# Kernel optimization log

Hardware: AMD Instinct MI355X
Metric: run time of the kernel (lower is better)

The kernel has to match this reference:

```python
import jax, jax.numpy as jnp
import numpy as np

S = 4096      # total packed tokens
B = 8         # number of variable-length segments
E = 1152      # embed_dim (SigLIP2 so400m)
H = 16        # num_heads
D = E // H    # head_dim = 72


def setup_inputs() -> dict:
    key = jax.random.key(0)
    ks = jax.random.split(key, 8)
    w_std = 0.02
    theta = jax.random.uniform(ks[1], (S, D), jnp.float32, 0.0, 2.0 * np.pi)
    return {
        "hidden_states": jax.random.normal(ks[0], (S, E), jnp.float32),
        "cu_seqlens": jnp.arange(B + 1, dtype=jnp.int32) * (S // B),
        "cos": jnp.cos(theta),
        "sin": jnp.sin(theta),
        "Wq": jax.random.normal(ks[2], (E, E), jnp.float32) * w_std,
        "bq": jnp.zeros((E,), jnp.float32),
        "Wk": jax.random.normal(ks[3], (E, E), jnp.float32) * w_std,
        "bk": jnp.zeros((E,), jnp.float32),
        "Wv": jax.random.normal(ks[4], (E, E), jnp.float32) * w_std,
        "bv": jnp.zeros((E,), jnp.float32),
        "Wo": jax.random.normal(ks[5], (E, E), jnp.float32) * w_std,
        "bo": jnp.zeros((E,), jnp.float32),
    }


def _rotate_half(x):
    x1, x2 = jnp.split(x, 2, axis=-1)
    return jnp.concatenate((-x2, x1), axis=-1)


def reference(hidden_states, cu_seqlens, cos, sin, Wq, bq, Wk, bk, Wv, bv, Wo, bo):
    seq_len = hidden_states.shape[0]
    scale = np.float32(D) ** -0.5
    # projections -> [S, H, D]
    q = (hidden_states @ Wq.T + bq).reshape(seq_len, H, D)
    k = (hidden_states @ Wk.T + bk).reshape(seq_len, H, D)
    v = (hidden_states @ Wv.T + bv).reshape(seq_len, H, D)
    # inline RoPE (apply_rotary_pos_emb_vision): cos/sin broadcast over heads
    c = cos[:, None, :]
    s = sin[:, None, :]
    q = q * c + _rotate_half(q) * s
    k = k * c + _rotate_half(k) * s
    # segment id per token from cu_seqlens; block-diagonal attention mask
    seg = jnp.searchsorted(cu_seqlens[1:], jnp.arange(seq_len, dtype=cu_seqlens.dtype), side="right")
    mask = seg[:, None] == seg[None, :]                     # [S, S]
    scores = jnp.einsum("shd,thd->hst", q, k) * scale       # [H, S, S]
    neg = jnp.finfo(scores.dtype).min
    scores = jnp.where(mask[None, :, :], scores, neg)
    probs = jax.nn.softmax(scores, axis=-1)
    attn = jnp.einsum("hst,thd->shd", probs, v).reshape(seq_len, E)
    return attn @ Wo.T + bo
```

## Files before the change

### kernel.cpp

```cpp
#include <hip/hip_runtime.h>
#include <float.h>

#define S_LEN 4096
#define E_DIM 1152
#define NH    16
#define HD    72
#define HD2   36
#define NQKV  3456

typedef __attribute__((ext_vector_type(4))) float f32x4;
typedef __attribute__((ext_vector_type(8))) _Float16 f16x8;

__device__ __forceinline__ unsigned short f2h(float f) {
    union { _Float16 h; unsigned short u; } c;
    c.h = (_Float16)f;
    return c.u;
}

__device__ __forceinline__ void gload_lds16(const unsigned short* g, unsigned short* l) {
    __builtin_amdgcn_global_load_lds(
        (const __attribute__((address_space(1))) unsigned int*)g,
        (__attribute__((address_space(3))) unsigned int*)l, 16, 0, 0);
}

__global__ __launch_bounds__(256)
void pack_f16(const float* __restrict__ hs, const float* __restrict__ wq,
              const float* __restrict__ wk, const float* __restrict__ wv,
              const float* __restrict__ wo,
              unsigned short* __restrict__ hs_h, unsigned short* __restrict__ wqkv_h,
              unsigned short* __restrict__ wo_h)
{
    const float* src; unsigned short* dst; int n4;
    const int WSZ = E_DIM * E_DIM;
    switch (blockIdx.z) {
        case 0: src = hs; dst = hs_h;             n4 = S_LEN * E_DIM / 4; break;
        case 1: src = wq; dst = wqkv_h;           n4 = WSZ / 4; break;
        case 2: src = wk; dst = wqkv_h + WSZ;     n4 = WSZ / 4; break;
        case 3: src = wv; dst = wqkv_h + 2 * WSZ; n4 = WSZ / 4; break;
        default: src = wo; dst = wo_h;            n4 = WSZ / 4; break;
    }
    for (int i = blockIdx.x * 256 + threadIdx.x; i < n4; i += gridDim.x * 256) {
        f32x4 x = ((const f32x4*)src)[i];
        ushort4 hv;
        hv.x = f2h(x[0]); hv.y = f2h(x[1]); hv.z = f2h(x[2]); hv.w = f2h(x[3]);
        ((ushort4*)dst)[i] = hv;
    }
}

__global__ __launch_bounds__(256, 4)
void gemm_qkv_f16(const unsigned short* __restrict__ Ah, const unsigned short* __restrict__ Wh,
                  const float* __restrict__ bq, const float* __restrict__ bk,
                  const float* __restrict__ bv,
                  float* __restrict__ oq, float* __restrict__ ok, float* __restrict__ ov)
{
    __shared__ unsigned short sA[128 * 64];
    __shared__ unsigned short sB[128 * 64];
    const int tid  = threadIdx.x;
    const int w    = tid >> 6, lane = tid & 63;
    const int quad = lane >> 4, m = lane & 15;
    const int wr   = w & 1,  wc = w >> 1;

    const int bid = blockIdx.x;
    const int lin = (bid & 7) * 108 + (bid >> 3);
    const int n_t = lin >> 5;
    const int m_t = lin & 31;
    const int m0  = m_t * 128;
    const int n0  = n_t * 128;

    const int srow = lane >> 3;
    const int skc  = (lane & 7) ^ srow;

    f32x4 acc[4][4];
    #pragma unroll
    for (int i = 0; i < 4; ++i)
        #pragma unroll
        for (int j = 0; j < 4; ++j) acc[i][j] = (f32x4){0.f, 0.f, 0.f, 0.f};

    const int rm7 = m & 7;

    for (int k0 = 0; k0 < E_DIM; k0 += 64) {
        #pragma unroll
        for (int c = 0; c < 4; ++c) {
            int r = 32 * w + 8 * c + srow;
            gload_lds16(Ah + (size_t)(m0 + r) * E_DIM + k0 + skc * 8, &sA[(32 * w + 8 * c) * 64]);
            gload_lds16(Wh + (size_t)(n0 + r) * E_DIM + k0 + skc * 8, &sB[(32 * w + 8 * c) * 64]);
        }
        __syncthreads();

        #pragma unroll
        for (int k3 = 0; k3 < 2; ++k3) {
            f16x8 ah[4], bh[4];
            #pragma unroll
            for (int t = 0; t < 4; ++t) {
                int pc = ((k3 << 2) + quad) ^ rm7;
                ah[t] = *(const f16x8*)&sA[(64 * wr + 16 * t + m) * 64 + pc * 8];
                bh[t] = *(const f16x8*)&sB[(64 * wc + 16 * t + m) * 64 + pc * 8];
            }
            #pragma unroll
            for (int rt = 0; rt < 4; ++rt)
                #pragma unroll
                for (int ct = 0; ct < 4; ++ct)
                    acc[rt][ct] = __builtin_amdgcn_mfma_f32_16x16x32_f16(ah[rt], bh[ct], acc[rt][ct], 0, 0, 0);
        }
        __syncthreads();
    }

    const int which = n0 / E_DIM;
    const int n0l = n0 - which * E_DIM;
    const float* bp = (which == 0) ? bq : (which == 1) ? bk : bv;
    float* Cp       = (which == 0) ? oq : (which == 1) ? ok : ov;
    #pragma unroll
    for (int ct = 0; ct < 4; ++ct) {
        int col = n0l + 64 * wc + 16 * ct + m;
        float bias = bp[col];
        #pragma unroll
        for (int rt = 0; rt < 4; ++rt)
            #pragma unroll
            for (int reg = 0; reg < 4; ++reg) {
                int row = m0 + 64 * wr + 16 * rt + 4 * quad + reg;
                Cp[(size_t)row * E_DIM + col] = acc[rt][ct][reg] + bias;
            }
    }
}

__global__ __launch_bounds__(256, 4)
void gemm_out_f16(const unsigned short* __restrict__ Ah, const unsigned short* __restrict__ Wh,
                  const float* __restrict__ bo, float* __restrict__ Cp)
{
    __shared__ unsigned short sA[64 * 64];
    __shared__ unsigned short sB[128 * 64];
    const int tid  = threadIdx.x;
    const int w    = tid >> 6, lane = tid & 63;
    const int quad = lane >> 4, m = lane & 15;
    const int m0   = blockIdx.y * 64;
    const int n0   = blockIdx.x * 128;

    const int srow = lane >> 3;
    const int skc  = (lane & 7) ^ srow;

    f32x4 acc[4][2];
    #pragma unroll
    for (int i = 0; i < 4; ++i)
        #pragma unroll
        for (int j = 0; j < 2; ++j) acc[i][j] = (f32x4){0.f, 0.f, 0.f, 0.f};

    const int rm7 = m & 7;

    for (int k0 = 0; k0 < E_DIM; k0 += 64) {
        #pragma unroll
        for (int c = 0; c < 2; ++c) {
            int r = 16 * w + 8 * c + srow;
            gload_lds16(Ah + (size_t)(m0 + r) * E_DIM + k0 + skc * 8, &sA[(16 * w + 8 * c) * 64]);
        }
        #pragma unroll
        for (int c = 0; c < 4; ++c) {
            int r = 32 * w + 8 * c + srow;
            gload_lds16(Wh + (size_t)(n0 + r) * E_DIM + k0 + skc * 8, &sB[(32 * w + 8 * c) * 64]);
        }
        __syncthreads();
        #pragma unroll
        for (int k3 = 0; k3 < 2; ++k3) {
            f16x8 ah[4], bh[2];
            int pc = ((k3 << 2) + quad) ^ rm7;
            #pragma unroll
            for (int t = 0; t < 4; ++t)
                ah[t] = *(const f16x8*)&sA[(16 * t + m) * 64 + pc * 8];
            #pragma unroll
            for (int ct = 0; ct < 2; ++ct)
                bh[ct] = *(const f16x8*)&sB[(32 * w + 16 * ct + m) * 64 + pc * 8];
            #pragma unroll
            for (int rt = 0; rt < 4; ++rt)
                #pragma unroll
                for (int ct = 0; ct < 2; ++ct)
                    acc[rt][ct] = __builtin_amdgcn_mfma_f32_16x16x32_f16(ah[rt], bh[ct], acc[rt][ct], 0, 0, 0);
        }
        __syncthreads();
    }

    #pragma unroll
    for (int ct = 0; ct < 2; ++ct) {
        int col = n0 + 32 * w + 16 * ct + m;
        float bias = bo[col];
        #pragma unroll
        for (int rt = 0; rt < 4; ++rt)
            #pragma unroll
            for (int reg = 0; reg < 4; ++reg) {
                int row = m0 + 16 * rt + 4 * quad + reg;
                Cp[(size_t)row * E_DIM + col] = acc[rt][ct][reg] + bias;
            }
    }
}

__global__ __launch_bounds__(256)
void vtrans(const float* __restrict__ v, unsigned short* __restrict__ vt)
{
    __shared__ unsigned short tile[HD][72];
    const int h = blockIdx.y;
    const int s0 = blockIdx.x * 64;
    for (int task = threadIdx.x; task < 64 * 18; task += 256) {
        int r = task / 18, c = task % 18;
        f32x4 x = *(const f32x4*)(v + (size_t)(s0 + r) * E_DIM + h * HD + (c << 2));
        tile[(c << 2) + 0][r] = f2h(x[0]);
        tile[(c << 2) + 1][r] = f2h(x[1]);
        tile[(c << 2) + 2][r] = f2h(x[2]);
        tile[(c << 2) + 3][r] = f2h(x[3]);
    }
    __syncthreads();
    for (int task = threadIdx.x; task < HD * 8; task += 256) {
        int d = task / 8, cc = task % 8;
        uint4 val = *(const uint4*)&tile[d][cc << 3];
        *(uint4*)(vt + ((size_t)h * HD + d) * S_LEN + s0 + (cc << 3)) = val;
    }
}

__global__ __launch_bounds__(256, 4)
void attn_rope(const float* __restrict__ qf, const float* __restrict__ kf,
               const float* __restrict__ cosb, const float* __restrict__ sinb,
               const unsigned short* __restrict__ vt, const int* __restrict__ cu,
               int nseg, unsigned short* __restrict__ out)
{
    __shared__ unsigned short ks_s[64][72];
    __shared__ unsigned short vs_s[80][72];
    __shared__ unsigned short ss_s[64][72];

    const int tid  = threadIdx.x;
    const int w    = tid >> 6;
    const int lane = tid & 63;
    const int quad = lane >> 4;
    const int m    = lane & 15;
    const int h    = blockIdx.y;
    const int qb0  = blockIdx.x * 64;
    const float scale = 0.11785113019775793f;

    {
        uint4 zz = make_uint4(0u, 0u, 0u, 0u);
        if (tid < 72) {
            int r = 72 + tid / 9, c = tid % 9;
            *(uint4*)&vs_s[r][c << 3] = zz;
        }
    }

    int rs_r[4], re_r[4];
    #pragma unroll
    for (int reg = 0; reg < 4; ++reg) {
        int row = qb0 + 16 * w + 4 * quad + reg;
        int st = 0;
        for (int i = 1; i < nseg; ++i) if (cu[i] <= row) st = i;
        rs_r[reg] = cu[st];
        re_r[reg] = cu[st + 1];
    }
    int st0 = 0, st1 = 0;
    for (int i = 1; i < nseg; ++i) {
        if (cu[i] <= qb0) st0 = i;
        if (cu[i] <= qb0 + 63) st1 = i;
    }
    const int kstart = cu[st0];
    const int kend   = cu[st1 + 1];

    for (int task = tid; task < 64 * 9; task += 256) {
        int row = task / 9, d0 = (task % 9) << 2;
        int s = qb0 + row;
        const float* xr = qf + (size_t)s * E_DIM + h * HD;
        f32x4 a  = *(const f32x4*)(xr + d0);
        f32x4 b  = *(const f32x4*)(xr + d0 + HD2);
        f32x4 c1 = *(const f32x4*)(cosb + (size_t)s * HD + d0);
        f32x4 s1 = *(const f32x4*)(sinb + (size_t)s * HD + d0);
        f32x4 c2 = *(const f32x4*)(cosb + (size_t)s * HD + d0 + HD2);
        f32x4 s2 = *(const f32x4*)(sinb + (size_t)s * HD + d0 + HD2);
        f32x4 r1 = a * c1 - b * s1;
        f32x4 r2 = b * c2 + a * s2;
        uint2 u1, u2;
        u1.x = (unsigned)f2h(r1[0]) | ((unsigned)f2h(r1[1]) << 16);
        u1.y = (unsigned)f2h(r1[2]) | ((unsigned)f2h(r1[3]) << 16);
        u2.x = (unsigned)f2h(r2[0]) | ((unsigned)f2h(r2[1]) << 16);
        u2.y = (unsigned)f2h(r2[2]) | ((unsigned)f2h(r2[3]) << 16);
        *(uint2*)&ks_s[row][d0]       = u1;
        *(uint2*)&ks_s[row][d0 + HD2] = u2;
    }
    __syncthreads();

    f16x8 qfr[3];
    {
        const unsigned short* qrow = &ks_s[16 * w + m][0];
        #pragma unroll
        for (int k3 = 0; k3 < 3; ++k3) {
            bool pad = (k3 == 2) && (quad != 0);
            int off = pad ? 0 : (k3 * 32 + quad * 8);
            f16x8 val = *(const f16x8*)(qrow + off);
            f16x8 z = {0, 0, 0, 0, 0, 0, 0, 0};
            qfr[k3] = pad ? z : val;
        }
    }

    f32x4 acc_o[5];
    #pragma unroll
    for (int i = 0; i < 5; ++i) acc_o[i] = (f32x4){0.f, 0.f, 0.f, 0.f};
    float l_r[4] = {0.f, 0.f, 0.f, 0.f};

    for (int kb_i = kstart; kb_i < kend; kb_i += 64) {
        __syncthreads();
        for (int task = tid; task < 64 * 9; task += 256) {
            int row = task / 9, d0 = (task % 9) << 2;
            int s = kb_i + row; if (s >= kend) s = kend - 1;
            const float* xr = kf + (size_t)s * E_DIM + h * HD;
            f32x4 a  = *(const f32x4*)(xr + d0);
            f32x4 b  = *(const f32x4*)(xr + d0 + HD2);
            f32x4 c1 = *(const f32x4*)(cosb + (size_t)s * HD + d0);
            f32x4 s1 = *(const f32x4*)(sinb + (size_t)s * HD + d0);
            f32x4 c2 = *(const f32x4*)(cosb + (size_t)s * HD + d0 + HD2);
            f32x4 s2 = *(const f32x4*)(sinb + (size_t)s * HD + d0 + HD2);
            f32x4 r1 = a * c1 - b * s1;
            f32x4 r2 = b * c2 + a * s2;
            uint2 u1, u2;
            u1.x = (unsigned)f2h(r1[0]) | ((unsigned)f2h(r1[1]) << 16);
            u1.y = (unsigned)f2h(r1[2]) | ((unsigned)f2h(r1[3]) << 16);
            u2.x = (unsigned)f2h(r2[0]) | ((unsigned)f2h(r2[1]) << 16);
            u2.y = (unsigned)f2h(r2[2]) | ((unsigned)f2h(r2[3]) << 16);
            *(uint2*)&ks_s[row][d0]       = u1;
            *(uint2*)&ks_s[row][d0 + HD2] = u2;
        }
        for (int slot = tid; slot < 72 * 8; slot += 256) {
            int d = slot / 8, c = slot % 8;
            int kk0 = kb_i + (c << 3);
            if (kk0 > S_LEN - 8) kk0 = S_LEN - 8;
            uint4 val = *(const uint4*)(vt + ((size_t)h * HD + d) * S_LEN + kk0);
            *(uint4*)&vs_s[d][c << 3] = val;
        }
        __syncthreads();

        f32x4 sacc[4];
        #pragma unroll
        for (int ct = 0; ct < 4; ++ct) sacc[ct] = (f32x4){0.f, 0.f, 0.f, 0.f};
        #pragma unroll
        for (int ct = 0; ct < 4; ++ct) {
            const unsigned short* krow = &ks_s[16 * ct + m][0];
            #pragma unroll
            for (int k3 = 0; k3 < 3; ++k3) {
                bool pad = (k3 == 2) && (quad != 0);
                int off = pad ? 0 : (k3 * 32 + quad * 8);
                f16x8 bfr = *(const f16x8*)(krow + off);
                f16x8 z = {0, 0, 0, 0, 0, 0, 0, 0};
                bfr = pad ? z : bfr;
                sacc[ct] = __builtin_amdgcn_mfma_f32_16x16x32_f16(qfr[k3], bfr, sacc[ct], 0, 0, 0);
            }
        }

        #pragma unroll
        for (int ct = 0; ct < 4; ++ct) {
            int key = kb_i + 16 * ct + m;
            #pragma unroll
            for (int reg = 0; reg < 4; ++reg) {
                bool valid = (key >= rs_r[reg]) && (key < re_r[reg]);
                float p = valid ? __expf(sacc[ct][reg] * scale) : 0.f;
                l_r[reg] += p;
                ss_s[16 * w + 4 * quad + reg][16 * ct + m] = f2h(p);
            }
        }

        {
            const unsigned short* prow = &ss_s[16 * w + m][0];
            f16x8 pf0 = *(const f16x8*)(prow + quad * 8);
            f16x8 pf1 = *(const f16x8*)(prow + 32 + quad * 8);
            #pragma unroll
            for (int ct2 = 0; ct2 < 5; ++ct2) {
                const unsigned short* vrow = &vs_s[16 * ct2 + m][0];
                f16x8 vf0 = *(const f16x8*)(vrow + quad * 8);
                f16x8 vf1 = *(const f16x8*)(vrow + 32 + quad * 8);
                acc_o[ct2] = __builtin_amdgcn_mfma_f32_16x16x32_f16(pf0, vf0, acc_o[ct2], 0, 0, 0);
                acc_o[ct2] = __builtin_amdgcn_mfma_f32_16x16x32_f16(pf1, vf1, acc_o[ct2], 0, 0, 0);
            }
        }
    }

    #pragma unroll
    for (int reg = 0; reg < 4; ++reg) {
        float l = l_r[reg];
        l += __shfl_xor(l, 1);
        l += __shfl_xor(l, 2);
        l += __shfl_xor(l, 4);
        l += __shfl_xor(l, 8);
        l_r[reg] = l;
    }

    #pragma unroll
    for (int reg = 0; reg < 4; ++reg) {
        float linv = (l_r[reg] > 0.f) ? 1.f / l_r[reg] : 0.f;
        int row = qb0 + 16 * w + 4 * quad + reg;
        unsigned short* orow = out + (size_t)row * E_DIM + h * HD;
        #pragma unroll
        for (int ct2 = 0; ct2 < 5; ++ct2) {
            int col = 16 * ct2 + m;
            if (col < HD) orow[col] = f2h(acc_o[ct2][reg] * linv);
        }
    }
}

extern "C" void kernel_launch(void* const* d_in, const int* in_sizes, int n_in,
                              void* d_out, int out_size, void* d_ws, size_t ws_size,
                              hipStream_t stream)
{
    const float* hs   = (const float*)d_in[0];
    const int*   cu   = (const int*)d_in[1];
    const float* cosb = (const float*)d_in[2];
    const float* sinb = (const float*)d_in[3];
    const float* Wq   = (const float*)d_in[4];
    const float* bq   = (const float*)d_in[5];
    const float* Wk   = (const float*)d_in[6];
    const float* bk   = (const float*)d_in[7];
    const float* Wv   = (const float*)d_in[8];
    const float* bv   = (const float*)d_in[9];
    const float* Wo   = (const float*)d_in[10];
    const float* bo   = (const float*)d_in[11];
    float* outp = (float*)d_out;

    const size_t mat = (size_t)S_LEN * E_DIM;
    float* qf = (float*)d_ws;
    float* kf = qf + mat;
    float* vf = kf + mat;
    unsigned short* hs_h   = (unsigned short*)(vf + mat);
    unsigned short* wqkv_h = hs_h + mat;
    unsigned short* wo_h   = wqkv_h + (size_t)NQKV * E_DIM;
    unsigned short* vtb    = wo_h + (size_t)E_DIM * E_DIM;
    unsigned short* attn_h = hs_h;

    const int nseg = in_sizes[1] - 1;

    dim3 gpack(512, 1, 5);
    pack_f16<<<gpack, 256, 0, stream>>>(hs, Wq, Wk, Wv, Wo, hs_h, wqkv_h, wo_h);

    gemm_qkv_f16<<<dim3(864), 256, 0, stream>>>(hs_h, wqkv_h, bq, bk, bv, qf, kf, vf);

    dim3 gvt(S_LEN / 64, NH, 1);
    vtrans<<<gvt, 256, 0, stream>>>(vf, vtb);

    dim3 gattn(S_LEN / 64, NH, 1);
    attn_rope<<<gattn, 256, 0, stream>>>(qf, kf, cosb, sinb, vtb, cu, nseg, attn_h);

    dim3 gout(E_DIM / 128, S_LEN / 64, 1);
    gemm_out_f16<<<gout, 256, 0, stream>>>(attn_h, wo_h, bo, outp);
}
```

Before: 227.5 us.

## Precompute RoPE'd fp16 K, register-prefetch K/V tiles, fast exp2 softmax

```diff
diff --git a/kernel.cpp b/kernel.cpp
--- a/kernel.cpp
+++ b/kernel.cpp
@@ -192,32 +192,59 @@
 }
 
 __global__ __launch_bounds__(256)
-void vtrans(const float* __restrict__ v, unsigned short* __restrict__ vt)
+void prep_kv(const float* __restrict__ kf, const float* __restrict__ vf,
+             const float* __restrict__ cosb, const float* __restrict__ sinb,
+             unsigned short* __restrict__ kh, unsigned short* __restrict__ vt)
 {
     __shared__ unsigned short tile[HD][72];
-    const int h = blockIdx.y;
+    const int h  = blockIdx.y;
     const int s0 = blockIdx.x * 64;
-    for (int task = threadIdx.x; task < 64 * 18; task += 256) {
-        int r = task / 18, c = task % 18;
-        f32x4 x = *(const f32x4*)(v + (size_t)(s0 + r) * E_DIM + h * HD + (c << 2));
-        tile[(c << 2) + 0][r] = f2h(x[0]);
-        tile[(c << 2) + 1][r] = f2h(x[1]);
-        tile[(c << 2) + 2][r] = f2h(x[2]);
-        tile[(c << 2) + 3][r] = f2h(x[3]);
-    }
-    __syncthreads();
-    for (int task = threadIdx.x; task < HD * 8; task += 256) {
-        int d = task / 8, cc = task % 8;
-        uint4 val = *(const uint4*)&tile[d][cc << 3];
-        *(uint4*)(vt + ((size_t)h * HD + d) * S_LEN + s0 + (cc << 3)) = val;
+
+    if (blockIdx.z == 0) {
+        for (int task = threadIdx.x; task < 64 * 9; task += 256) {
+            int row = task / 9, d0 = (task % 9) << 2;
+            int s = s0 + row;
+            const float* xr = kf + (size_t)s * E_DIM + h * HD;
+            f32x4 a  = *(const f32x4*)(xr + d0);
+            f32x4 b  = *(const f32x4*)(xr + d0 + HD2);
+            f32x4 c1 = *(const f32x4*)(cosb + (size_t)s * HD + d0);
+            f32x4 s1 = *(const f32x4*)(sinb + (size_t)s * HD + d0);
+            f32x4 c2 = *(const f32x4*)(cosb + (size_t)s * HD + d0 + HD2);
+            f32x4 s2 = *(const f32x4*)(sinb + (size_t)s * HD + d0 + HD2);
+            f32x4 r1 = a * c1 - b * s1;
+            f32x4 r2 = b * c2 + a * s2;
+            uint2 u1, u2;
+            u1.x = (unsigned)f2h(r1[0]) | ((unsigned)f2h(r1[1]) << 16);
+            u1.y = (unsigned)f2h(r1[2]) | ((unsigned)f2h(r1[3]) << 16);
+            u2.x = (unsigned)f2h(r2[0]) | ((unsigned)f2h(r2[1]) << 16);
+            u2.y = (unsigned)f2h(r2[2]) | ((unsigned)f2h(r2[3]) << 16);
+            unsigned short* orow = kh + ((size_t)h * S_LEN + s) * HD;
+            *(uint2*)&orow[d0]       = u1;
+            *(uint2*)&orow[d0 + HD2] = u2;
+        }
+    } else {
+        for (int task = threadIdx.x; task < 64 * 18; task += 256) {
+            int r = task / 18, c = task % 18;
+            f32x4 x = *(const f32x4*)(vf + (size_t)(s0 + r) * E_DIM + h * HD + (c << 2));
+            tile[(c << 2) + 0][r] = f2h(x[0]);
+            tile[(c << 2) + 1][r] = f2h(x[1]);
+            tile[(c << 2) + 2][r] = f2h(x[2]);
+            tile[(c << 2) + 3][r] = f2h(x[3]);
+        }
+        __syncthreads();
+        for (int task = threadIdx.x; task < HD * 8; task += 256) {
+            int d = task / 8, cc = task % 8;
+            uint4 val = *(const uint4*)&tile[d][cc << 3];
+            *(uint4*)(vt + ((size_t)h * HD + d) * S_LEN + s0 + (cc << 3)) = val;
+        }
     }
 }
 
 __global__ __launch_bounds__(256, 4)
-void attn_rope(const float* __restrict__ qf, const float* __restrict__ kf,
-               const float* __restrict__ cosb, const float* __restrict__ sinb,
-               const unsigned short* __restrict__ vt, const int* __restrict__ cu,
-               int nseg, unsigned short* __restrict__ out)
+void attn_f16(const float* __restrict__ qf, const float* __restrict__ cosb,
+              const float* __restrict__ sinb, const unsigned short* __restrict__ kh,
+              const unsigned short* __restrict__ vt, const int* __restrict__ cu,
+              int nseg, unsigned short* __restrict__ out)
 {
     __shared__ unsigned short ks_s[64][72];
     __shared__ unsigned short vs_s[80][72];
@@ -230,7 +257,7 @@
     const int m    = lane & 15;
     const int h    = blockIdx.y;
     const int qb0  = blockIdx.x * 64;
-    const float scale = 0.11785113019775793f;
+    const float cexp = 0.17002324f;
 
     {
         uint4 zz = make_uint4(0u, 0u, 0u, 0u);
@@ -256,6 +283,28 @@
     }
     const int kstart = cu[st0];
     const int kend   = cu[st1 + 1];
+    const bool aligned = (st0 == st1);
+
+    const unsigned short* ktbase = kh + (size_t)h * S_LEN * HD;
+    const unsigned short* vtbase = vt + (size_t)h * HD * S_LEN;
+    unsigned short* ksf = &ks_s[0][0];
+
+    const int sl0 = tid, sl1 = tid + 256;
+    const int sl2 = (tid < 64) ? tid + 512 : tid + 256;
+    const int vd0 = sl0 >> 3, vc0 = (sl0 & 7) << 3;
+    const int vd1 = sl1 >> 3, vc1 = (sl1 & 7) << 3;
+    const int vd2 = sl2 >> 3, vc2 = (sl2 & 7) << 3;
+
+    uint4 kp0, kp1, kp2, vp0, vp1, vp2;
+    {
+        const unsigned short* kt = ktbase + (size_t)kstart * HD;
+        kp0 = *(const uint4*)(kt + sl0 * 8);
+        kp1 = *(const uint4*)(kt + sl1 * 8);
+        kp2 = *(const uint4*)(kt + sl2 * 8);
+        vp0 = *(const uint4*)(vtbase + (size_t)vd0 * S_LEN + kstart + vc0);
+        vp1 = *(const uint4*)(vtbase + (size_t)vd1 * S_LEN + kstart + vc1);
+        vp2 = *(const uint4*)(vtbase + (size_t)vd2 * S_LEN + kstart + vc2);
+    }
 
     for (int task = tid; task < 64 * 9; task += 256) {
         int row = task / 9, d0 = (task % 9) << 2;
@@ -297,36 +346,26 @@
     for (int i = 0; i < 5; ++i) acc_o[i] = (f32x4){0.f, 0.f, 0.f, 0.f};
     float l_r[4] = {0.f, 0.f, 0.f, 0.f};
 
-    for (int kb_i = kstart; kb_i < kend; kb_i += 64) {
-        __syncthreads();
-        for (int task = tid; task < 64 * 9; task += 256) {
-            int row = task / 9, d0 = (task % 9) << 2;
-            int s = kb_i + row; if (s >= kend) s = kend - 1;
-            const float* xr = kf + (size_t)s * E_DIM + h * HD;
-            f32x4 a  = *(const f32x4*)(xr + d0);
-            f32x4 b  = *(const f32x4*)(xr + d0 + HD2);
-            f32x4 c1 = *(const f32x4*)(cosb + (size_t)s * HD + d0);
-            f32x4 s1 = *(const f32x4*)(sinb + (size_t)s * HD + d0);
-            f32x4 c2 = *(const f32x4*)(cosb + (size_t)s * HD + d0 + HD2);
-            f32x4 s2 = *(const f32x4*)(sinb + (size_t)s * HD + d0 + HD2);
-            f32x4 r1 = a * c1 - b * s1;
-            f32x4 r2 = b * c2 + a * s2;
-            uint2 u1, u2;
-            u1.x = (unsigned)f2h(r1[0]) | ((unsigned)f2h(r1[1]) << 16);
-            u1.y = (unsigned)f2h(r1[2]) | ((unsigned)f2h(r1[3]) << 16);
-            u2.x = (unsigned)f2h(r2[0]) | ((unsigned)f2h(r2[1]) << 16);
-            u2.y = (unsigned)f2h(r2[2]) | ((unsigned)f2h(r2[3]) << 16);
-            *(uint2*)&ks_s[row][d0]       = u1;
-            *(uint2*)&ks_s[row][d0 + HD2] = u2;
-        }
-        for (int slot = tid; slot < 72 * 8; slot += 256) {
-            int d = slot / 8, c = slot % 8;
-            int kk0 = kb_i + (c << 3);
-            if (kk0 > S_LEN - 8) kk0 = S_LEN - 8;
-            uint4 val = *(const uint4*)(vt + ((size_t)h * HD + d) * S_LEN + kk0);
-            *(uint4*)&vs_s[d][c << 3] = val;
-        }
-        __syncthreads();
+    for (int kb = kstart; kb < kend; kb += 64) {
+        __syncthreads();
+        *(uint4*)(ksf + sl0 * 8) = kp0;
+        *(uint4*)(ksf + sl1 * 8) = kp1;
+        if (tid < 64) *(uint4*)(ksf + sl2 * 8) = kp2;
+        *(uint4*)&vs_s[vd0][vc0] = vp0;
+        *(uint4*)&vs_s[vd1][vc1] = vp1;
+        if (tid < 64) *(uint4*)&vs_s[vd2][vc2] = vp2;
+        __syncthreads();
+
+        int kn = kb + 64;
+        if (kn < kend) {
+            const unsigned short* kt = ktbase + (size_t)kn * HD;
+            kp0 = *(const uint4*)(kt + sl0 * 8);
+            kp1 = *(const uint4*)(kt + sl1 * 8);
+            kp2 = *(const uint4*)(kt + sl2 * 8);
+            vp0 = *(const uint4*)(vtbase + (size_t)vd0 * S_LEN + kn + vc0);
+            vp1 = *(const uint4*)(vtbase + (size_t)vd1 * S_LEN + kn + vc1);
+            vp2 = *(const uint4*)(vtbase + (size_t)vd2 * S_LEN + kn + vc2);
+        }
 
         f32x4 sacc[4];
         #pragma unroll
@@ -345,15 +384,26 @@
             }
         }
 
-        #pragma unroll
-        for (int ct = 0; ct < 4; ++ct) {
-            int key = kb_i + 16 * ct + m;
-            #pragma unroll
-            for (int reg = 0; reg < 4; ++reg) {
-                bool valid = (key >= rs_r[reg]) && (key < re_r[reg]);
-                float p = valid ? __expf(sacc[ct][reg] * scale) : 0.f;
-                l_r[reg] += p;
-                ss_s[16 * w + 4 * quad + reg][16 * ct + m] = f2h(p);
+        if (aligned) {
+            #pragma unroll
+            for (int ct = 0; ct < 4; ++ct)
+                #pragma unroll
+                for (int reg = 0; reg < 4; ++reg) {
+                    float p = __builtin_amdgcn_exp2f(sacc[ct][reg] * cexp);
+                    l_r[reg] += p;
+                    ss_s[16 * w + 4 * quad + reg][16 * ct + m] = f2h(p);
+                }
+        } else {
+            #pragma unroll
+            for (int ct = 0; ct < 4; ++ct) {
+                int key = kb + 16 * ct + m;
+                #pragma unroll
+                for (int reg = 0; reg < 4; ++reg) {
+                    bool valid = (key >= rs_r[reg]) && (key < re_r[reg]);
+                    float p = valid ? __builtin_amdgcn_exp2f(sacc[ct][reg] * cexp) : 0.f;
+                    l_r[reg] += p;
+                    ss_s[16 * w + 4 * quad + reg][16 * ct + m] = f2h(p);
+                }
             }
         }
 
@@ -421,7 +471,8 @@
     unsigned short* wqkv_h = hs_h + mat;
     unsigned short* wo_h   = wqkv_h + (size_t)NQKV * E_DIM;
     unsigned short* vtb    = wo_h + (size_t)E_DIM * E_DIM;
-    unsigned short* attn_h = hs_h;
+    unsigned short* kh     = hs_h;
+    unsigned short* attn_h = (unsigned short*)vf;
 
     const int nseg = in_sizes[1] - 1;
 
@@ -430,11 +481,11 @@
 
     gemm_qkv_f16<<<dim3(864), 256, 0, stream>>>(hs_h, wqkv_h, bq, bk, bv, qf, kf, vf);
 
-    dim3 gvt(S_LEN / 64, NH, 1);
-    vtrans<<<gvt, 256, 0, stream>>>(vf, vtb);
+    dim3 gprep(S_LEN / 64, NH, 2);
+    prep_kv<<<gprep, 256, 0, stream>>>(kf, vf, cosb, sinb, kh, vtb);
 
     dim3 gattn(S_LEN / 64, NH, 1);
-    attn_rope<<<gattn, 256, 0, stream>>>(qf, kf, cosb, sinb, vtb, cu, nseg, attn_h);
+    attn_f16<<<gattn, 256, 0, stream>>>(qf, cosb, sinb, kh, vtb, cu, nseg, attn_h);
 
     dim3 gout(E_DIM / 128, S_LEN / 64, 1);
     gemm_out_f16<<<gout, 256, 0, stream>>>(attn_h, wo_h, bo, outp);
```

After: 208.7 us. -8.3%, faster.
